# Optimization experiments

Hardware: AMD Instinct MI355X
Metric: run time of the kernel (lower is better)

The kernel has to match this reference:

```python
import jax, jax.numpy as jnp
import numpy as np

B, S, H, D = 2, 2048, 16, 64

def setup_inputs() -> dict:
    key = jax.random.key(0)
    kq, kk, kv = jax.random.split(key, 3)
    q = jax.random.normal(kq, (B, S, H, D), dtype=jnp.float32)
    k = jax.random.normal(kk, (B, S, H, D), dtype=jnp.float32)
    v = jax.random.normal(kv, (B, S, H, D), dtype=jnp.float32)
    return {"q": q, "k": k, "v": v}

def reference(q, k, v):
    # q, k, v: [B, S, H, D]; single-process path == full softmax attention,
    # which is exactly what the ring online-softmax computes over all chunks.
    d = q.shape[-1]
    scale = 1.0 / jnp.sqrt(jnp.asarray(d, dtype=q.dtype))
    # scores: [B, H, Sq, Sk]
    scores = jnp.einsum("bqhd,bkhd->bhqk", q, k) * scale
    attn = jax.nn.softmax(scores, axis=-1)
    # output back in [B, S, H, D] layout (torch transposes back)
    out = jnp.einsum("bhqk,bkhd->bqhd", attn, v)
    return out
```

## Files before the change

### kernel.cpp

```cpp
#include <hip/hip_runtime.h>
#include <hip/hip_bf16.h>

namespace {

constexpr int Sseq = 2048;
constexpr int NH   = 16;
constexpr int HD   = 64;
constexpr int ROW  = NH * HD;
constexpr int BM   = 128;
constexpr int BN   = 64;
constexpr int MT   = 2;
constexpr int NT   = Sseq / BN;
constexpr float QSCALE = 0.18033688011112042f;

typedef __bf16 bf16_t;
typedef __attribute__((ext_vector_type(8))) bf16_t bf16x8;
typedef __attribute__((ext_vector_type(4))) float f32x4;
typedef __attribute__((ext_vector_type(2))) unsigned int u32x2;
typedef __attribute__((ext_vector_type(4))) unsigned int u32x4;

union Frag { bf16x8 v; unsigned int u[4]; };

__device__ inline unsigned int pkbf(float a, float b) {
  union { __hip_bfloat162 h; unsigned int u; } x;
  x.h = __float22bfloat162_rn(make_float2(a, b));
  return x.u;
}


__global__ __launch_bounds__(256)
void fa_fwd(const float* __restrict__ Q, const float* __restrict__ K,
            const float* __restrict__ V, float* __restrict__ O) {
  const int id   = blockIdx.x;
  const int bh   = id & 31;
  const int qblk = id >> 5;
  const int tid  = threadIdx.x;
  const int wave = tid >> 6;
  const int lane = tid & 63;
  const int qd   = lane >> 4;
  const int lm   = lane & 15;

  const size_t base = (size_t)(bh >> 4) * Sseq * ROW + (size_t)(bh & 15) * HD;
  const float* qb = Q + base;
  const float* kb = K + base;
  const float* vb = V + base;
  float*       ob = O + base;

  __shared__ __align__(16) unsigned short KT[2][HD * 64];
  __shared__ __align__(16) unsigned short VT[2][HD * 64];
  __shared__ __align__(16) unsigned short PB[4][MT][16 * 64];

  const int qrow0 = qblk * BM + wave * (MT * 16);

  Frag qf[MT][2];
  for (int mt = 0; mt < MT; ++mt) {
    const float* qp = qb + (size_t)(qrow0 + mt * 16 + lm) * ROW;
    for (int ks = 0; ks < 2; ++ks) {
      f32x4 a = *(const f32x4*)(qp + ks * 32 + qd * 8);
      f32x4 c = *(const f32x4*)(qp + ks * 32 + qd * 8 + 4);
      qf[mt][ks].u[0] = pkbf(a[0] * QSCALE, a[1] * QSCALE);
      qf[mt][ks].u[1] = pkbf(a[2] * QSCALE, a[3] * QSCALE);
      qf[mt][ks].u[2] = pkbf(c[0] * QSCALE, c[1] * QSCALE);
      qf[mt][ks].u[3] = pkbf(c[2] * QSCALE, c[3] * QSCALE);
    }
  }

  f32x4 oacc[MT][4] = {};
  float lsum[MT] = {};

  const int kr = tid >> 2;
  const int kd = (tid & 3) * 16;
  const int n4 = (tid & 15) * 4;
  const int d4 = (tid >> 4) * 4;

  const float* kp = kb + (size_t)kr * ROW + kd;
  const float* vp = vb + (size_t)n4 * ROW + d4;

  f32x4 kx0 = *(const f32x4*)(kp);
  f32x4 kx1 = *(const f32x4*)(kp + 4);
  f32x4 kx2 = *(const f32x4*)(kp + 8);
  f32x4 kx3 = *(const f32x4*)(kp + 12);
  f32x4 vx0 = *(const f32x4*)(vp);
  f32x4 vx1 = *(const f32x4*)(vp + ROW);
  f32x4 vx2 = *(const f32x4*)(vp + 2 * ROW);
  f32x4 vx3 = *(const f32x4*)(vp + 3 * ROW);

  for (int t = 0; t < NT; ++t) {
    unsigned short* kt = KT[t & 1];
    unsigned short* vt = VT[t & 1];

    {
      int c0 = ((tid & 3) * 2) ^ (kr & 7);
      int c1 = ((tid & 3) * 2 + 1) ^ (kr & 7);
      u32x4 w0, w1;
      w0.x = pkbf(kx0[0], kx0[1]); w0.y = pkbf(kx0[2], kx0[3]);
      w0.z = pkbf(kx1[0], kx1[1]); w0.w = pkbf(kx1[2], kx1[3]);
      w1.x = pkbf(kx2[0], kx2[1]); w1.y = pkbf(kx2[2], kx2[3]);
      w1.z = pkbf(kx3[0], kx3[1]); w1.w = pkbf(kx3[2], kx3[3]);
      *(u32x4*)(kt + kr * 64 + c0 * 8) = w0;
      *(u32x4*)(kt + kr * 64 + c1 * 8) = w1;
    }
    {
      #pragma unroll
      for (int i = 0; i < 4; ++i) {
        int d = d4 + i;
        int chunk = (n4 >> 3) ^ (d & 7);
        u32x2 val; val.x = pkbf(vx0[i], vx1[i]); val.y = pkbf(vx2[i], vx3[i]);
        *(u32x2*)(vt + d * 64 + chunk * 8 + (n4 & 7)) = val;
      }
    }

    __syncthreads();

    if (t + 1 < NT) {
      kp += BN * ROW; vp += BN * ROW;
      kx0 = *(const f32x4*)(kp);
      kx1 = *(const f32x4*)(kp + 4);
      kx2 = *(const f32x4*)(kp + 8);
      kx3 = *(const f32x4*)(kp + 12);
      vx0 = *(const f32x4*)(vp);
      vx1 = *(const f32x4*)(vp + ROW);
      vx2 = *(const f32x4*)(vp + 2 * ROW);
      vx3 = *(const f32x4*)(vp + 3 * ROW);
    }

    #pragma unroll
    for (int c = 0; c < 4; ++c) {
      Frag kf0, kf1;
      {
        int r = c * 16 + lm;
        int ch0 = (qd) ^ (lm & 7);
        int ch1 = (4 + qd) ^ (lm & 7);
        kf0.v = *(const bf16x8*)(kt + r * 64 + ch0 * 8);
        kf1.v = *(const bf16x8*)(kt + r * 64 + ch1 * 8);
      }
      #pragma unroll
      for (int mt = 0; mt < MT; ++mt) {
        f32x4 s = {};
        s = __builtin_amdgcn_mfma_f32_16x16x32_bf16(kf0.v, qf[mt][0].v, s, 0, 0, 0);
        s = __builtin_amdgcn_mfma_f32_16x16x32_bf16(kf1.v, qf[mt][1].v, s, 0, 0, 0);
        float e0 = __builtin_amdgcn_exp2f(s[0]);
        float e1 = __builtin_amdgcn_exp2f(s[1]);
        float e2 = __builtin_amdgcn_exp2f(s[2]);
        float e3 = __builtin_amdgcn_exp2f(s[3]);
        lsum[mt] += (e0 + e1) + (e2 + e3);
        int n = c * 16 + qd * 4;
        int chunk = (n >> 3) ^ (lm & 7);
        u32x2 val; val.x = pkbf(e0, e1); val.y = pkbf(e2, e3);
        *(u32x2*)(PB[wave][mt] + lm * 64 + chunk * 8 + (n & 7)) = val;
      }
    }

    __threadfence_block();

    #pragma unroll
    for (int ks = 0; ks < 2; ++ks) {
      bf16x8 pfr[MT];
      #pragma unroll
      for (int mt = 0; mt < MT; ++mt) {
        int chunk = (ks * 4 + qd) ^ (lm & 7);
        pfr[mt] = *(const bf16x8*)(PB[wave][mt] + lm * 64 + chunk * 8);
      }
      #pragma unroll
      for (int dt = 0; dt < 4; ++dt) {
        int d = dt * 16 + lm;
        int chunk = (ks * 4 + qd) ^ (d & 7);
        bf16x8 vf = *(const bf16x8*)(vt + d * 64 + chunk * 8);
        #pragma unroll
        for (int mt = 0; mt < MT; ++mt)
          oacc[mt][dt] = __builtin_amdgcn_mfma_f32_16x16x32_bf16(vf, pfr[mt], oacc[mt][dt], 0, 0, 0);
      }
    }
  }

  #pragma unroll
  for (int mt = 0; mt < MT; ++mt) {
    float l = lsum[mt];
    l += __shfl_xor(l, 16, 64);
    l += __shfl_xor(l, 32, 64);
    float r = 1.0f / l;
    float* op = ob + (size_t)(qrow0 + mt * 16 + lm) * ROW + qd * 4;
    #pragma unroll
    for (int dt = 0; dt < 4; ++dt) {
      f32x4 o = oacc[mt][dt];
      o[0] *= r; o[1] *= r; o[2] *= r; o[3] *= r;
      *(f32x4*)(op + dt * 16) = o;
    }
  }
}

}

extern "C" void kernel_launch(void* const* d_in, const int* in_sizes, int n_in,
                              void* d_out, int out_size, void* d_ws, size_t ws_size,
                              hipStream_t stream) {
  const float* q = (const float*)d_in[0];
  const float* k = (const float*)d_in[1];
  const float* v = (const float*)d_in[2];
  float* o = (float*)d_out;
  (void)in_sizes; (void)n_in; (void)out_size; (void)d_ws; (void)ws_size;
  dim3 grid(2 * NH * (Sseq / BM));
  dim3 block(256);
  hipLaunchKernelGGL(fa_fwd, grid, block, 0, stream, q, k, v, o);
}
```

Baseline: 148.7 us.

## Deepen global prefetch to two K/V tiles ahead with register double-buffering

Keeps two sets of K/V prefetch registers so global loads for tile t+2 are issued while tile t is computed, unrolling the loop by two over the two LDS buffers. The aim is to hide more global-memory latency behind the MFMA and softmax work. It adds 32 more VGPRs for the in-flight tiles, which could lower occupancy or cause spills.

```diff
diff --git a/kernel.cpp b/kernel.cpp
--- a/kernel.cpp
+++ b/kernel.cpp
@@ -73,30 +73,36 @@
   const int n4 = (tid & 15) * 4;
   const int d4 = (tid >> 4) * 4;
 
-  const float* kp = kb + (size_t)kr * ROW + kd;
-  const float* vp = vb + (size_t)n4 * ROW + d4;
-
-  f32x4 kx0 = *(const f32x4*)(kp);
-  f32x4 kx1 = *(const f32x4*)(kp + 4);
-  f32x4 kx2 = *(const f32x4*)(kp + 8);
-  f32x4 kx3 = *(const f32x4*)(kp + 12);
-  f32x4 vx0 = *(const f32x4*)(vp);
-  f32x4 vx1 = *(const f32x4*)(vp + ROW);
-  f32x4 vx2 = *(const f32x4*)(vp + 2 * ROW);
-  f32x4 vx3 = *(const f32x4*)(vp + 3 * ROW);
-
-  for (int t = 0; t < NT; ++t) {
-    unsigned short* kt = KT[t & 1];
-    unsigned short* vt = VT[t & 1];
-
+  const float* kpA = kb + (size_t)kr * ROW + kd;
+  const float* vpA = vb + (size_t)n4 * ROW + d4;
+  const float* kpB = kpA + (size_t)BN * ROW;
+  const float* vpB = vpA + (size_t)BN * ROW;
+
+  f32x4 ka[4], va[4], kB[4], vB[4];
+
+  auto ldK = [&](const float* p, f32x4* r) {
+    r[0] = *(const f32x4*)(p);
+    r[1] = *(const f32x4*)(p + 4);
+    r[2] = *(const f32x4*)(p + 8);
+    r[3] = *(const f32x4*)(p + 12);
+  };
+  auto ldV = [&](const float* p, f32x4* r) {
+    r[0] = *(const f32x4*)(p);
+    r[1] = *(const f32x4*)(p + ROW);
+    r[2] = *(const f32x4*)(p + 2 * ROW);
+    r[3] = *(const f32x4*)(p + 3 * ROW);
+  };
+
+  auto stage = [&](unsigned short* kt, unsigned short* vt,
+                   const f32x4* kx, const f32x4* vx) {
     {
       int c0 = ((tid & 3) * 2) ^ (kr & 7);
       int c1 = ((tid & 3) * 2 + 1) ^ (kr & 7);
       u32x4 w0, w1;
-      w0.x = pkbf(kx0[0], kx0[1]); w0.y = pkbf(kx0[2], kx0[3]);
-      w0.z = pkbf(kx1[0], kx1[1]); w0.w = pkbf(kx1[2], kx1[3]);
-      w1.x = pkbf(kx2[0], kx2[1]); w1.y = pkbf(kx2[2], kx2[3]);
-      w1.z = pkbf(kx3[0], kx3[1]); w1.w = pkbf(kx3[2], kx3[3]);
+      w0.x = pkbf(kx[0][0], kx[0][1]); w0.y = pkbf(kx[0][2], kx[0][3]);
+      w0.z = pkbf(kx[1][0], kx[1][1]); w0.w = pkbf(kx[1][2], kx[1][3]);
+      w1.x = pkbf(kx[2][0], kx[2][1]); w1.y = pkbf(kx[2][2], kx[2][3]);
+      w1.z = pkbf(kx[3][0], kx[3][1]); w1.w = pkbf(kx[3][2], kx[3][3]);
       *(u32x4*)(kt + kr * 64 + c0 * 8) = w0;
       *(u32x4*)(kt + kr * 64 + c1 * 8) = w1;
     }
@@ -105,25 +111,13 @@
       for (int i = 0; i < 4; ++i) {
         int d = d4 + i;
         int chunk = (n4 >> 3) ^ (d & 7);
-        u32x2 val; val.x = pkbf(vx0[i], vx1[i]); val.y = pkbf(vx2[i], vx3[i]);
+        u32x2 val; val.x = pkbf(vx[0][i], vx[1][i]); val.y = pkbf(vx[2][i], vx[3][i]);
         *(u32x2*)(vt + d * 64 + chunk * 8 + (n4 & 7)) = val;
       }
     }
-
-    __syncthreads();
-
-    if (t + 1 < NT) {
-      kp += BN * ROW; vp += BN * ROW;
-      kx0 = *(const f32x4*)(kp);
-      kx1 = *(const f32x4*)(kp + 4);
-      kx2 = *(const f32x4*)(kp + 8);
-      kx3 = *(const f32x4*)(kp + 12);
-      vx0 = *(const f32x4*)(vp);
-      vx1 = *(const f32x4*)(vp + ROW);
-      vx2 = *(const f32x4*)(vp + 2 * ROW);
-      vx3 = *(const f32x4*)(vp + 3 * ROW);
-    }
-
+  };
+
+  auto compute = [&](const unsigned short* kt, const unsigned short* vt) {
     #pragma unroll
     for (int c = 0; c < 4; ++c) {
       Frag kf0, kf1;
@@ -171,6 +165,27 @@
           oacc[mt][dt] = __builtin_amdgcn_mfma_f32_16x16x32_bf16(vf, pfr[mt], oacc[mt][dt], 0, 0, 0);
       }
     }
+  };
+
+  ldK(kpA, ka); ldV(vpA, va);
+  ldK(kpB, kB); ldV(vpB, vB);
+
+  for (int t = 0; t < NT; t += 2) {
+    stage(KT[0], VT[0], ka, va);
+    __syncthreads();
+    if (t + 2 < NT) {
+      kpA += (size_t)2 * BN * ROW; vpA += (size_t)2 * BN * ROW;
+      ldK(kpA, ka); ldV(vpA, va);
+    }
+    compute(KT[0], VT[0]);
+
+    stage(KT[1], VT[1], kB, vB);
+    __syncthreads();
+    if (t + 3 < NT) {
+      kpB += (size_t)2 * BN * ROW; vpB += (size_t)2 * BN * ROW;
+      ldK(kpB, kB); ldV(vpB, vB);
+    }
+    compute(KT[1], VT[1]);
   }
 
   #pragma unroll
```

Measured after the change: 141.0 us. 5.2% less time.

## Pre-convert K/V to swizzled bf16 tiles and DMA them into LDS

Applied to the files above, without the earlier changes.

Adds a prep kernel that converts K and V once into bf16, pre-swizzled 16KB tile images in the workspace. The main kernel then streams each tile straight into LDS with global_load_lds, double-buffered, so the per-block fp32 loads and conversion of K/V inside the loop go away. The query tile per block is halved to 64 rows (one 16-row tile per wave) with launch bounds raised for occupancy, so there are more blocks. The cost is an extra kernel launch and a workspace round trip, and the old kernel is kept as a fallback when the workspace is too small.

```diff
diff --git a/kernel.cpp b/kernel.cpp
--- a/kernel.cpp
+++ b/kernel.cpp
@@ -7,10 +7,11 @@
 constexpr int NH   = 16;
 constexpr int HD   = 64;
 constexpr int ROW  = NH * HD;
-constexpr int BM   = 128;
 constexpr int BN   = 64;
-constexpr int MT   = 2;
 constexpr int NT   = Sseq / BN;
+constexpr int BMm  = 64;
+constexpr size_t IMG_BYTES = 16384;
+constexpr size_t WS_NEED   = (size_t)32 * NT * IMG_BYTES;
 constexpr float QSCALE = 0.18033688011112042f;
 
 typedef __bf16 bf16_t;
@@ -27,10 +28,68 @@
   return x.u;
 }
 
+__device__ inline void dma16(const void* g, void* l) {
+  __builtin_amdgcn_global_load_lds(
+      (const __attribute__((address_space(1))) void*)g,
+      (__attribute__((address_space(3))) void*)l, 16, 0, 0);
+}
+
 
 __global__ __launch_bounds__(256)
-void fa_fwd(const float* __restrict__ Q, const float* __restrict__ K,
-            const float* __restrict__ V, float* __restrict__ O) {
+void prep_kv(const float* __restrict__ K, const float* __restrict__ V,
+             unsigned short* __restrict__ ws) {
+  const int id  = blockIdx.x;
+  const int bh  = id & 31;
+  const int t   = id >> 5;
+  const int tid = threadIdx.x;
+
+  const size_t base = (size_t)(bh >> 4) * Sseq * ROW + (size_t)(bh & 15) * HD
+                    + (size_t)(t * BN) * ROW;
+  const float* kb = K + base;
+  const float* vb = V + base;
+
+  unsigned short* gK = (unsigned short*)((char*)ws + (size_t)(bh * NT + t) * IMG_BYTES);
+  unsigned short* gV = gK + 4096;
+
+  {
+    const int kr = tid >> 2;
+    const int kd = (tid & 3) * 16;
+    const float* p = kb + (size_t)kr * ROW + kd;
+    f32x4 x0 = *(const f32x4*)(p);
+    f32x4 x1 = *(const f32x4*)(p + 4);
+    f32x4 x2 = *(const f32x4*)(p + 8);
+    f32x4 x3 = *(const f32x4*)(p + 12);
+    int c0 = ((tid & 3) * 2) ^ (kr & 7);
+    int c1 = ((tid & 3) * 2 + 1) ^ (kr & 7);
+    u32x4 w0, w1;
+    w0.x = pkbf(x0[0], x0[1]); w0.y = pkbf(x0[2], x0[3]);
+    w0.z = pkbf(x1[0], x1[1]); w0.w = pkbf(x1[2], x1[3]);
+    w1.x = pkbf(x2[0], x2[1]); w1.y = pkbf(x2[2], x2[3]);
+    w1.z = pkbf(x3[0], x3[1]); w1.w = pkbf(x3[2], x3[3]);
+    *(u32x4*)(gK + kr * 64 + c0 * 8) = w0;
+    *(u32x4*)(gK + kr * 64 + c1 * 8) = w1;
+  }
+  {
+    const int n4 = (tid & 15) * 4;
+    const int d4 = (tid >> 4) * 4;
+    const float* p = vb + (size_t)n4 * ROW + d4;
+    f32x4 r0 = *(const f32x4*)(p);
+    f32x4 r1 = *(const f32x4*)(p + ROW);
+    f32x4 r2 = *(const f32x4*)(p + 2 * ROW);
+    f32x4 r3 = *(const f32x4*)(p + 3 * ROW);
+    #pragma unroll
+    for (int i = 0; i < 4; ++i) {
+      int d = d4 + i;
+      int chunk = (n4 >> 3) ^ (d & 7);
+      u32x2 val; val.x = pkbf(r0[i], r1[i]); val.y = pkbf(r2[i], r3[i]);
+      *(u32x2*)(gV + d * 64 + chunk * 8 + (n4 & 7)) = val;
+    }
+  }
+}
+
+__global__ __launch_bounds__(256, 4)
+void fa_main(const float* __restrict__ Q, const unsigned short* __restrict__ ws,
+             float* __restrict__ O) {
   const int id   = blockIdx.x;
   const int bh   = id & 31;
   const int qblk = id >> 5;
@@ -42,13 +101,128 @@
 
   const size_t base = (size_t)(bh >> 4) * Sseq * ROW + (size_t)(bh & 15) * HD;
   const float* qb = Q + base;
+  float*       ob = O + base;
+  const char*  imgs = (const char*)ws + (size_t)bh * NT * IMG_BYTES;
+
+  __shared__ __align__(16) unsigned short KV[2][8192];
+  __shared__ __align__(16) unsigned short PB[4][16 * 64];
+
+  const int qrow0 = qblk * BMm + wave * 16;
+
+  Frag qf[2];
+  {
+    const float* qp = qb + (size_t)(qrow0 + lm) * ROW;
+    for (int ks = 0; ks < 2; ++ks) {
+      f32x4 a = *(const f32x4*)(qp + ks * 32 + qd * 8);
+      f32x4 c = *(const f32x4*)(qp + ks * 32 + qd * 8 + 4);
+      qf[ks].u[0] = pkbf(a[0] * QSCALE, a[1] * QSCALE);
+      qf[ks].u[1] = pkbf(a[2] * QSCALE, a[3] * QSCALE);
+      qf[ks].u[2] = pkbf(c[0] * QSCALE, c[1] * QSCALE);
+      qf[ks].u[3] = pkbf(c[2] * QSCALE, c[3] * QSCALE);
+    }
+  }
+
+  f32x4 oacc[4] = {};
+  float lsum = 0.f;
+
+  auto dma_tile = [&](int t, int b) {
+    const char* img = imgs + (size_t)t * IMG_BYTES;
+    char* dst = (char*)&KV[b][0];
+    int woff = wave * 1024;
+    #pragma unroll
+    for (int j = 0; j < 4; ++j)
+      dma16(img + j * 4096 + woff + lane * 16, dst + j * 4096 + woff);
+  };
+
+  dma_tile(0, 0);
+
+  for (int t = 0; t < NT; ++t) {
+    __syncthreads();
+    if (t + 1 < NT) dma_tile(t + 1, (t + 1) & 1);
+
+    const unsigned short* kt = &KV[t & 1][0];
+    const unsigned short* vt = &KV[t & 1][4096];
+
+    #pragma unroll
+    for (int c = 0; c < 4; ++c) {
+      Frag kf0, kf1;
+      {
+        int r = c * 16 + lm;
+        int ch0 = (qd) ^ (lm & 7);
+        int ch1 = (4 + qd) ^ (lm & 7);
+        kf0.v = *(const bf16x8*)(kt + r * 64 + ch0 * 8);
+        kf1.v = *(const bf16x8*)(kt + r * 64 + ch1 * 8);
+      }
+      f32x4 s = {};
+      s = __builtin_amdgcn_mfma_f32_16x16x32_bf16(kf0.v, qf[0].v, s, 0, 0, 0);
+      s = __builtin_amdgcn_mfma_f32_16x16x32_bf16(kf1.v, qf[1].v, s, 0, 0, 0);
+      float e0 = __builtin_amdgcn_exp2f(s[0]);
+      float e1 = __builtin_amdgcn_exp2f(s[1]);
+      float e2 = __builtin_amdgcn_exp2f(s[2]);
+      float e3 = __builtin_amdgcn_exp2f(s[3]);
+      lsum += (e0 + e1) + (e2 + e3);
+      int n = c * 16 + qd * 4;
+      int chunk = (n >> 3) ^ (lm & 7);
+      u32x2 val; val.x = pkbf(e0, e1); val.y = pkbf(e2, e3);
+      *(u32x2*)(PB[wave] + lm * 64 + chunk * 8 + (n & 7)) = val;
+    }
+
+    __threadfence_block();
+
+    #pragma unroll
+    for (int ks = 0; ks < 2; ++ks) {
+      bf16x8 pfr;
+      {
+        int chunk = (ks * 4 + qd) ^ (lm & 7);
+        pfr = *(const bf16x8*)(PB[wave] + lm * 64 + chunk * 8);
+      }
+      #pragma unroll
+      for (int dt = 0; dt < 4; ++dt) {
+        int d = dt * 16 + lm;
+        int chunk = (ks * 4 + qd) ^ (d & 7);
+        bf16x8 vf = *(const bf16x8*)(vt + d * 64 + chunk * 8);
+        oacc[dt] = __builtin_amdgcn_mfma_f32_16x16x32_bf16(vf, pfr, oacc[dt], 0, 0, 0);
+      }
+    }
+  }
+
+  {
+    float l = lsum;
+    l += __shfl_xor(l, 16, 64);
+    l += __shfl_xor(l, 32, 64);
+    float r = 1.0f / l;
+    float* op = ob + (size_t)(qrow0 + lm) * ROW + qd * 4;
+    #pragma unroll
+    for (int dt = 0; dt < 4; ++dt) {
+      f32x4 o = oacc[dt];
+      o[0] *= r; o[1] *= r; o[2] *= r; o[3] *= r;
+      *(f32x4*)(op + dt * 16) = o;
+    }
+  }
+}
+
+__global__ __launch_bounds__(256)
+void fa_fwd_fb(const float* __restrict__ Q, const float* __restrict__ K,
+               const float* __restrict__ V, float* __restrict__ O) {
+  constexpr int BM = 128, MT = 2;
+  const int id   = blockIdx.x;
+  const int bh   = id & 31;
+  const int qblk = id >> 5;
+  const int tid  = threadIdx.x;
+  const int wave = tid >> 6;
+  const int lane = tid & 63;
+  const int qd   = lane >> 4;
+  const int lm   = lane & 15;
+
+  const size_t base = (size_t)(bh >> 4) * Sseq * ROW + (size_t)(bh & 15) * HD;
+  const float* qb = Q + base;
   const float* kb = K + base;
   const float* vb = V + base;
   float*       ob = O + base;
 
   __shared__ __align__(16) unsigned short KT[2][HD * 64];
   __shared__ __align__(16) unsigned short VT[2][HD * 64];
-  __shared__ __align__(16) unsigned short PB[4][MT][16 * 64];
+  __shared__ __align__(16) unsigned short PBf[4][MT][16 * 64];
 
   const int qrow0 = qblk * BM + wave * (MT * 16);
 
@@ -147,7 +321,7 @@
         int n = c * 16 + qd * 4;
         int chunk = (n >> 3) ^ (lm & 7);
         u32x2 val; val.x = pkbf(e0, e1); val.y = pkbf(e2, e3);
-        *(u32x2*)(PB[wave][mt] + lm * 64 + chunk * 8 + (n & 7)) = val;
+        *(u32x2*)(PBf[wave][mt] + lm * 64 + chunk * 8 + (n & 7)) = val;
       }
     }
 
@@ -159,7 +333,7 @@
       #pragma unroll
       for (int mt = 0; mt < MT; ++mt) {
         int chunk = (ks * 4 + qd) ^ (lm & 7);
-        pfr[mt] = *(const bf16x8*)(PB[wave][mt] + lm * 64 + chunk * 8);
+        pfr[mt] = *(const bf16x8*)(PBf[wave][mt] + lm * 64 + chunk * 8);
       }
       #pragma unroll
       for (int dt = 0; dt < 4; ++dt) {
@@ -198,8 +372,14 @@
   const float* k = (const float*)d_in[1];
   const float* v = (const float*)d_in[2];
   float* o = (float*)d_out;
-  (void)in_sizes; (void)n_in; (void)out_size; (void)d_ws; (void)ws_size;
-  dim3 grid(2 * NH * (Sseq / BM));
-  dim3 block(256);
-  hipLaunchKernelGGL(fa_fwd, grid, block, 0, stream, q, k, v, o);
-}
+  (void)in_sizes; (void)n_in; (void)out_size;
+  if (ws_size >= WS_NEED) {
+    hipLaunchKernelGGL(prep_kv, dim3(32 * NT), dim3(256), 0, stream,
+                       k, v, (unsigned short*)d_ws);
+    hipLaunchKernelGGL(fa_main, dim3(32 * (Sseq / BMm)), dim3(256), 0, stream,
+                       q, (const unsigned short*)d_ws, o);
+  } else {
+    hipLaunchKernelGGL(fa_fwd_fb, dim3(2 * NH * (Sseq / 128)), dim3(256), 0, stream,
+                       q, k, v, o);
+  }
+}
```

New measurement: 141.6 us. -4.8%, faster.
